# Kernel tuning notes

Hardware: AMD Instinct MI355X
Metric: run time of the kernel (lower is better)

The kernel has to match this reference:

```python
import jax, jax.numpy as jnp
import numpy as np
import math

B, N = 2, 384
TF, POS, TIME = 22, 32, 32
TPROJ = TIME + 1  # embed_fixed appends frame_mask channel
CS, CZ = 256, 128
POS_MAX, TIME_MAX = 2056.0, 10000.0
LN_EPS = 1e-5


def _index_emb(idx):
    # sinusoidal positional embedding of integer indices -> [..., POS]
    K = jnp.arange(POS // 2, dtype=jnp.float32)
    ang = idx[..., None].astype(jnp.float32) * jnp.pi / (POS_MAX ** (2.0 * K / POS))
    return jnp.concatenate([jnp.sin(ang), jnp.cos(ang)], axis=-1)


def _time_emb(t):
    # standard score-sde timestep embedding -> [M, TIME]
    half = TIME // 2
    freqs = jnp.exp(-(math.log(TIME_MAX) / (half - 1)) * jnp.arange(half, dtype=jnp.float32))
    ang = t[:, None] * freqs[None, :]
    return jnp.concatenate([jnp.sin(ang), jnp.cos(ang)], axis=-1)


def _ln(x, g, b):
    m = jnp.mean(x, axis=-1, keepdims=True)
    v = jnp.var(x, axis=-1, keepdims=True)
    return (x - m) * jax.lax.rsqrt(v + LN_EPS) * g + b


def _lin(x, W, b):
    return x @ W.T + b


def _forward(seq_idx, seq_feat, timestep, frame_mask,
             W_npos, b_npos, W_ntf, b_ntf, W_ntime, b_ntime,
             W_n1, b_n1, W_n2, b_n2, g_n, be_n,
             W_epos, b_epos, W_etf, b_etf, W_etime, b_etime,
             W_e1, b_e1, W_e2, b_e2, g_e, be_e):
    Bn, Nn = seq_idx.shape
    rel = seq_idx[:, :, None] - seq_idx[:, None, :]  # [B,N,N]
    seq_emb = _lin(_index_emb(seq_idx), W_npos, b_npos)          # [B,N,CS]
    edge_emb = _lin(_index_emb(rel), W_epos, b_epos)             # [B,N,N,CZ]
    seq_emb = seq_emb + _lin(seq_feat, W_ntf, b_ntf)
    # _cross_concat(x) @ W^T == (x @ Wl^T)[:, :, None] + (x @ Wr^T)[:, None, :] + b
    # (same math, avoids the O(N^2 * 2*TF) concatenated intermediate)
    edge_emb = edge_emb + (seq_feat @ W_etf[:, :TF].T)[:, :, None, :] \
                        + (seq_feat @ W_etf[:, TF:].T)[:, None, :, :] + b_etf
    t_res = (timestep[:, None] * frame_mask).reshape(-1)
    temb = _time_emb(t_res).reshape(Bn, Nn, TIME)
    temb = jnp.concatenate([temb, frame_mask[..., None]], axis=-1)  # embed_fixed -> TPROJ
    seq_emb = seq_emb + _lin(temb, W_ntime, b_ntime)
    edge_emb = edge_emb + (temb @ W_etime[:, :TPROJ].T)[:, :, None, :] \
                        + (temb @ W_etime[:, TPROJ:].T)[:, None, :, :] + b_etime
    # node_embedder: ReLU -> Linear -> ReLU -> Linear -> LayerNorm
    h = _lin(jax.nn.relu(seq_emb), W_n1, b_n1)
    seq_emb = _ln(_lin(jax.nn.relu(h), W_n2, b_n2), g_n, be_n)
    h = _lin(jax.nn.relu(edge_emb), W_e1, b_e1)
    edge_emb = _ln(_lin(jax.nn.relu(h), W_e2, b_e2), g_e, be_e)
    return seq_emb, edge_emb


def setup_inputs() -> dict:
    key = jax.random.key(0)
    ks = jax.random.split(key, 20)
    inp = {
        'seq_idx': jnp.sort(jax.random.randint(ks[0], (B, N), 0, 1000), axis=-1),
        'seq_feat': jax.random.normal(ks[1], (B, N, TF), dtype=jnp.float32),
        'timestep': jax.random.uniform(ks[2], (B,), dtype=jnp.float32),
        'frame_mask': jnp.ones((B, N), dtype=jnp.float32),
    }
    def lin(k, o, i):
        return 0.02 * jax.random.normal(k, (o, i), dtype=jnp.float32), jnp.zeros((o,), jnp.float32)
    inp['W_npos'], inp['b_npos'] = lin(ks[3], CS, POS)
    inp['W_ntf'], inp['b_ntf'] = lin(ks[4], CS, TF)
    inp['W_ntime'], inp['b_ntime'] = lin(ks[5], CS, TPROJ)
    inp['W_n1'], inp['b_n1'] = lin(ks[6], CS, CS)
    inp['W_n2'], inp['b_n2'] = lin(ks[7], CS, CS)
    inp['g_n'], inp['be_n'] = jnp.ones((CS,), jnp.float32), jnp.zeros((CS,), jnp.float32)
    inp['W_epos'], inp['b_epos'] = lin(ks[8], CZ, POS)
    inp['W_etf'], inp['b_etf'] = lin(ks[9], CZ, 2 * TF)
    inp['W_etime'], inp['b_etime'] = lin(ks[10], CZ, 2 * TPROJ)
    inp['W_e1'], inp['b_e1'] = lin(ks[11], CZ, CZ)
    inp['W_e2'], inp['b_e2'] = lin(ks[12], CZ, CZ)
    inp['g_e'], inp['be_e'] = jnp.ones((CZ,), jnp.float32), jnp.zeros((CZ,), jnp.float32)
    return inp


def reference(seq_idx, seq_feat, timestep, frame_mask,
              W_npos, b_npos, W_ntf, b_ntf, W_ntime, b_ntime,
              W_n1, b_n1, W_n2, b_n2, g_n, be_n,
              W_epos, b_epos, W_etf, b_etf, W_etime, b_etime,
              W_e1, b_e1, W_e2, b_e2, g_e, be_e):
    return _forward(seq_idx, seq_feat, timestep, frame_mask,
                    W_npos, b_npos, W_ntf, b_ntf, W_ntime, b_ntime,
                    W_n1, b_n1, W_n2, b_n2, g_n, be_n,
                    W_epos, b_epos, W_etf, b_etf, W_etime, b_etime,
                    W_e1, b_e1, W_e2, b_e2, g_e, be_e)
```

## Files before the change

kernel.cpp:

```cpp
#include <hip/hip_runtime.h>
#include <hip/hip_bf16.h>

#define BB 2
#define NN 384
#define TFD 22
#define POSD 32
#define TPROJ 33
#define CS 256
#define CZ 128
#define PI_F 3.14159265358979323846f

typedef __hip_bfloat16 bf16;
typedef __attribute__((ext_vector_type(8))) short short8;
typedef __attribute__((ext_vector_type(4))) float floatx4;

__device__ __forceinline__ float bfbits2f(unsigned short u) {
  unsigned v = ((unsigned)u) << 16;
  float f;
  __builtin_memcpy(&f, &v, 4);
  return f;
}
__device__ __forceinline__ unsigned short f2bf(float x) {
  bf16 h = __float2bfloat16(x);
  unsigned short u;
  __builtin_memcpy(&u, &h, 2);
  return u;
}
__device__ __forceinline__ bool probe_f32(const void* fm) {
  return *(const unsigned*)fm == 0x3F800000u;
}

#define TAB_OFF 0
#define SEQ0_OFF 262144
#define EL_OFF 458752
#define ER_OFF 557056
#define P_OFF 655360
#define WB_OFF 716288
#define pSEQF 0
#define pTS 16896
#define pFM 16898
#define pWNPOS 17666
#define pBNPOS 25858
#define pWNTF 26114
#define pBNTF 31746
#define pWNTIME 32002
#define pBNTIME 40450
#define pBN1 40706
#define pBN2 40962
#define pGN 41218
#define pBEN 41474
#define pWEPOS 41730
#define pBEPOS 45826
#define pWETF 45954
#define pBETF 51586
#define pWETIME 51714
#define pBETIME 60162
#define pBE1 60290
#define pBE2 60418
#define pGE 60546
#define pBEE 60674
#define UB_WE1 0
#define UB_WE2 16384
#define UB_WN1 32768
#define UB_WN2 98304

struct InPtrs { const void* p[28]; };

__global__ void cvt_all(InPtrs ip, float* __restrict__ ws) {
  const int idx = blockIdx.x * 256 + threadIdx.x;
  if (idx >= 224642) return;
  const int srci[27] = {1,2,3,4,5,6,7,8,9,11,13,14,15,16,17,18,19,20,21,23,25,26,27,22,24,10,12};
  const int pre[28] = {0,16896,16898,17666,25858,26114,31746,32002,40450,40706,40962,41218,41474,
                       41730,45826,45954,51586,51714,60162,60290,60418,60546,60674,60802,
                       77186,93570,159106,224642};
  const bool f32 = probe_f32(ip.p[3]);
  int e = 0;
  while (idx >= pre[e + 1]) ++e;
  const int j = idx - pre[e];
  const void* sp = ip.p[srci[e]];
  if (e < 23) {
    float v = f32 ? ((const float*)sp)[j] : bfbits2f(((const unsigned short*)sp)[j]);
    ws[P_OFF + pre[e] + j] = v;
  } else {
    const int ub[4] = {UB_WE1, UB_WE2, UB_WN1, UB_WN2};
    unsigned short* wb = (unsigned short*)(ws + WB_OFF);
    wb[ub[e - 23] + j] = f32 ? f2bf(((const float*)sp)[j]) : ((const unsigned short*)sp)[j];
  }
}

__global__ void tab_kernel(float* __restrict__ ws) {
  const float* P = ws + P_OFF;
  __shared__ float pe[POSD];
  int r = blockIdx.x, t = threadIdx.x;
  if (t < 16) {
    float ang = (float)(r - 1024) * PI_F * powf(2056.0f, -(float)t * (1.0f / 16.0f));
    pe[t] = sinf(ang);
    pe[t + 16] = cosf(ang);
  }
  __syncthreads();
  float acc = P[pBEPOS + t] + P[pBETF + t] + P[pBETIME + t];
  const float* w = P + pWEPOS + t * POSD;
#pragma unroll
  for (int k = 0; k < POSD; ++k) acc += pe[k] * w[k];
  ws[TAB_OFF + r * CZ + t] = acc;
}

__global__ void nodeprep(const int* __restrict__ seq_idx, float* __restrict__ ws) {
  const float* P = ws + P_OFF;
  __shared__ float pe[POSD];
  __shared__ float temb[TPROJ];
  __shared__ float sf[TFD];
  int bn = blockIdx.x, t = threadIdx.x;
  int b = bn / NN;
  float fm = P[pFM + bn];
  if (t < 16) {
    float idxv = (float)seq_idx[bn];
    float ang = idxv * PI_F * powf(2056.0f, -(float)t * (1.0f / 16.0f));
    pe[t] = sinf(ang);
    pe[t + 16] = cosf(ang);
    float tres = P[pTS + b] * fm;
    float freq = expf(-(logf(10000.0f) * (1.0f / 15.0f)) * (float)t);
    temb[t] = sinf(tres * freq);
    temb[t + 16] = cosf(tres * freq);
  }
  if (t == 16) temb[32] = fm;
  if (t < TFD) sf[t] = P[pSEQF + bn * TFD + t];
  __syncthreads();
  {
    int c = t;
    float acc = P[pBNPOS + c] + P[pBNTF + c] + P[pBNTIME + c];
    const float* w = P + pWNPOS + c * POSD;
#pragma unroll
    for (int k = 0; k < POSD; ++k) acc += pe[k] * w[k];
    const float* w2 = P + pWNTF + c * TFD;
#pragma unroll
    for (int k = 0; k < TFD; ++k) acc += sf[k] * w2[k];
    const float* w3 = P + pWNTIME + c * TPROJ;
#pragma unroll
    for (int k = 0; k < TPROJ; ++k) acc += temb[k] * w3[k];
    ws[SEQ0_OFF + bn * CS + c] = acc;
  }
  if (t < CZ) {
    int c = t;
    float acc = 0.0f;
    const float* w = P + pWETF + c * (2 * TFD);
#pragma unroll
    for (int k = 0; k < TFD; ++k) acc += sf[k] * w[k];
    const float* w2 = P + pWETIME + c * (2 * TPROJ);
#pragma unroll
    for (int k = 0; k < TPROJ; ++k) acc += temb[k] * w2[k];
    ws[EL_OFF + bn * CZ + c] = acc;
  } else {
    int c = t - CZ;
    float acc = 0.0f;
    const float* w = P + pWETF + c * (2 * TFD) + TFD;
#pragma unroll
    for (int k = 0; k < TFD; ++k) acc += sf[k] * w[k];
    const float* w2 = P + pWETIME + c * (2 * TPROJ) + TPROJ;
#pragma unroll
    for (int k = 0; k < TPROJ; ++k) acc += temb[k] * w2[k];
    ws[ER_OFF + bn * CZ + c] = acc;
  }
}

__global__ __launch_bounds__(256) void node_mfma(const float* __restrict__ ws,
                                                 const void* __restrict__ fmraw,
                                                 void* __restrict__ outv) {
  __shared__ __align__(16) unsigned short sA0[32][CS + 8];
  __shared__ __align__(16) unsigned short sA1[32][CS + 8];
  __shared__ float sO[32][CS + 4];
  __shared__ float sRed[32][8], sRedQ[32][8], sMu[32], sRs[32];
  const float* P = ws + P_OFF;
  const unsigned short* WB = (const unsigned short*)(ws + WB_OFF);
  const unsigned short* W1 = WB + UB_WN1;
  const unsigned short* W2 = WB + UB_WN2;
  const int row0 = blockIdx.x * 32;
  const int t = threadIdx.x;
  const int wave = t >> 6, lane = t & 63, quad = lane >> 4, l16 = lane & 15;
  {
    const float* seq0 = ws + SEQ0_OFF;
#pragma unroll
    for (int r = 0; r < 32; ++r) sA0[r][t] = f2bf(fmaxf(seq0[(row0 + r) * CS + t], 0.0f));
  }
  __syncthreads();
  short8 af[2][8];
  floatx4 acc[2][4];
#pragma unroll
  for (int mt = 0; mt < 2; ++mt)
#pragma unroll
    for (int ks = 0; ks < 8; ++ks)
      af[mt][ks] = *(const short8*)&sA0[mt * 16 + l16][ks * 32 + quad * 8];
#pragma unroll
  for (int mt = 0; mt < 2; ++mt)
#pragma unroll
    for (int n = 0; n < 4; ++n) acc[mt][n] = (floatx4){0.f, 0.f, 0.f, 0.f};
#pragma unroll
  for (int ntl = 0; ntl < 4; ++ntl) {
    int n0 = (wave * 4 + ntl) * 16;
#pragma unroll
    for (int ks = 0; ks < 8; ++ks) {
      short8 bfr = *(const short8*)&W1[(n0 + l16) * CS + ks * 32 + quad * 8];
      acc[0][ntl] = __builtin_amdgcn_mfma_f32_16x16x32_bf16(af[0][ks], bfr, acc[0][ntl], 0, 0, 0);
      acc[1][ntl] = __builtin_amdgcn_mfma_f32_16x16x32_bf16(af[1][ks], bfr, acc[1][ntl], 0, 0, 0);
    }
  }
#pragma unroll
  for (int ntl = 0; ntl < 4; ++ntl) {
    int n0 = (wave * 4 + ntl) * 16;
    float b1v = P[pBN1 + n0 + l16];
#pragma unroll
    for (int mt = 0; mt < 2; ++mt)
#pragma unroll
      for (int i = 0; i < 4; ++i)
        sA1[mt * 16 + quad * 4 + i][n0 + l16] = f2bf(fmaxf(acc[mt][ntl][i] + b1v, 0.0f));
  }
  __syncthreads();
#pragma unroll
  for (int mt = 0; mt < 2; ++mt)
#pragma unroll
    for (int ks = 0; ks < 8; ++ks)
      af[mt][ks] = *(const short8*)&sA1[mt * 16 + l16][ks * 32 + quad * 8];
#pragma unroll
  for (int mt = 0; mt < 2; ++mt)
#pragma unroll
    for (int n = 0; n < 4; ++n) acc[mt][n] = (floatx4){0.f, 0.f, 0.f, 0.f};
#pragma unroll
  for (int ntl = 0; ntl < 4; ++ntl) {
    int n0 = (wave * 4 + ntl) * 16;
#pragma unroll
    for (int ks = 0; ks < 8; ++ks) {
      short8 bfr = *(const short8*)&W2[(n0 + l16) * CS + ks * 32 + quad * 8];
      acc[0][ntl] = __builtin_amdgcn_mfma_f32_16x16x32_bf16(af[0][ks], bfr, acc[0][ntl], 0, 0, 0);
      acc[1][ntl] = __builtin_amdgcn_mfma_f32_16x16x32_bf16(af[1][ks], bfr, acc[1][ntl], 0, 0, 0);
    }
  }
#pragma unroll
  for (int ntl = 0; ntl < 4; ++ntl) {
    int n0 = (wave * 4 + ntl) * 16;
    float b2v = P[pBN2 + n0 + l16];
#pragma unroll
    for (int mt = 0; mt < 2; ++mt)
#pragma unroll
      for (int i = 0; i < 4; ++i)
        sO[mt * 16 + quad * 4 + i][n0 + l16] = acc[mt][ntl][i] + b2v;
  }
  __syncthreads();
  {
    int r = t >> 3, seg = t & 7;
    float s = 0.f, q = 0.f;
#pragma unroll
    for (int k = 0; k < 32; ++k) { float v = sO[r][seg * 32 + k]; s += v; q += v * v; }
    sRed[r][seg] = s; sRedQ[r][seg] = q;
  }
  __syncthreads();
  if (t < 32) {
    float s = 0.f, q = 0.f;
#pragma unroll
    for (int k = 0; k < 8; ++k) { s += sRed[t][k]; q += sRedQ[t][k]; }
    float mu = s * (1.0f / CS);
    float var = q * (1.0f / CS) - mu * mu;
    sMu[t] = mu; sRs[t] = rsqrtf(var + 1e-5f);
  }
  __syncthreads();
  {
    float g = P[pGN + t], be = P[pBEN + t];
    if (probe_f32(fmraw)) {
      float* o = (float*)outv;
#pragma unroll
      for (int r = 0; r < 32; ++r)
        o[(size_t)(row0 + r) * CS + t] = (sO[r][t] - sMu[r]) * sRs[r] * g + be;
    } else {
      bf16* o = (bf16*)outv;
#pragma unroll
      for (int r = 0; r < 32; ++r)
        o[(size_t)(row0 + r) * CS + t] = __float2bfloat16((sO[r][t] - sMu[r]) * sRs[r] * g + be);
    }
  }
}

__global__ __launch_bounds__(256) void edge_mfma(const int* __restrict__ seq_idx,
                                                 const float* __restrict__ ws,
                                                 const void* __restrict__ fmraw,
                                                 void* __restrict__ outv) {
  __shared__ __align__(16) unsigned short sA0[32][CZ + 8];
  __shared__ __align__(16) unsigned short sA1[32][CZ + 8];
  __shared__ float sO[32][CZ + 4];
  __shared__ int sRel[32];
  __shared__ float sRed[32][8], sRedQ[32][8], sMu[32], sRs[32];
  const float* tab = ws + TAB_OFF;
  const float* eL = ws + EL_OFF;
  const float* eR = ws + ER_OFF;
  const float* P = ws + P_OFF;
  const unsigned short* WB = (const unsigned short*)(ws + WB_OFF);
  const unsigned short* W1 = WB + UB_WE1;
  const unsigned short* W2 = WB + UB_WE2;
  const int bid = blockIdx.x;
  const int jt = bid % (NN / 32);
  const int rem = bid / (NN / 32);
  const int irow = rem % NN;
  const int b = rem / NN;
  const int j0 = jt * 32;
  const int t = threadIdx.x;
  const int wave = t >> 6, lane = t & 63, quad = lane >> 4, l16 = lane & 15;
  if (t < 32) {
    int rel = seq_idx[b * NN + irow] - seq_idx[b * NN + j0 + t] + 1024;
    sRel[t] = min(max(rel, 0), 2047);
  }
  __syncthreads();
  {
    int c = t & 127, rh = (t >> 7) * 16;
    float eLi = eL[(b * NN + irow) * CZ + c];
#pragma unroll
    for (int rr = 0; rr < 16; ++rr) {
      int r = rh + rr;
      float v = tab[sRel[r] * CZ + c] + eLi + eR[(b * NN + j0 + r) * CZ + c];
      sA0[r][c] = f2bf(fmaxf(v, 0.0f));
    }
  }
  __syncthreads();
  short8 af[2][4];
  floatx4 acc[2][2];
#pragma unroll
  for (int mt = 0; mt < 2; ++mt)
#pragma unroll
    for (int ks = 0; ks < 4; ++ks)
      af[mt][ks] = *(const short8*)&sA0[mt * 16 + l16][ks * 32 + quad * 8];
#pragma unroll
  for (int mt = 0; mt < 2; ++mt)
#pragma unroll
    for (int n = 0; n < 2; ++n) acc[mt][n] = (floatx4){0.f, 0.f, 0.f, 0.f};
#pragma unroll
  for (int ntl = 0; ntl < 2; ++ntl) {
    int n0 = (wave * 2 + ntl) * 16;
#pragma unroll
    for (int ks = 0; ks < 4; ++ks) {
      short8 bfr = *(const short8*)&W1[(n0 + l16) * CZ + ks * 32 + quad * 8];
      acc[0][ntl] = __builtin_amdgcn_mfma_f32_16x16x32_bf16(af[0][ks], bfr, acc[0][ntl], 0, 0, 0);
      acc[1][ntl] = __builtin_amdgcn_mfma_f32_16x16x32_bf16(af[1][ks], bfr, acc[1][ntl], 0, 0, 0);
    }
  }
#pragma unroll
  for (int ntl = 0; ntl < 2; ++ntl) {
    int n0 = (wave * 2 + ntl) * 16;
    float b1v = P[pBE1 + n0 + l16];
#pragma unroll
    for (int mt = 0; mt < 2; ++mt)
#pragma unroll
      for (int i = 0; i < 4; ++i)
        sA1[mt * 16 + quad * 4 + i][n0 + l16] = f2bf(fmaxf(acc[mt][ntl][i] + b1v, 0.0f));
  }
  __syncthreads();
#pragma unroll
  for (int mt = 0; mt < 2; ++mt)
#pragma unroll
    for (int ks = 0; ks < 4; ++ks)
      af[mt][ks] = *(const short8*)&sA1[mt * 16 + l16][ks * 32 + quad * 8];
#pragma unroll
  for (int mt = 0; mt < 2; ++mt)
#pragma unroll
    for (int n = 0; n < 2; ++n) acc[mt][n] = (floatx4){0.f, 0.f, 0.f, 0.f};
#pragma unroll
  for (int ntl = 0; ntl < 2; ++ntl) {
    int n0 = (wave * 2 + ntl) * 16;
#pragma unroll
    for (int ks = 0; ks < 4; ++ks) {
      short8 bfr = *(const short8*)&W2[(n0 + l16) * CZ + ks * 32 + quad * 8];
      acc[0][ntl] = __builtin_amdgcn_mfma_f32_16x16x32_bf16(af[0][ks], bfr, acc[0][ntl], 0, 0, 0);
      acc[1][ntl] = __builtin_amdgcn_mfma_f32_16x16x32_bf16(af[1][ks], bfr, acc[1][ntl], 0, 0, 0);
    }
  }
#pragma unroll
  for (int ntl = 0; ntl < 2; ++ntl) {
    int n0 = (wave * 2 + ntl) * 16;
    float b2v = P[pBE2 + n0 + l16];
#pragma unroll
    for (int mt = 0; mt < 2; ++mt)
#pragma unroll
      for (int i = 0; i < 4; ++i)
        sO[mt * 16 + quad * 4 + i][n0 + l16] = acc[mt][ntl][i] + b2v;
  }
  __syncthreads();
  {
    int r = t >> 3, seg = t & 7;
    float s = 0.f, q = 0.f;
#pragma unroll
    for (int k = 0; k < 16; ++k) { float v = sO[r][seg * 16 + k]; s += v; q += v * v; }
    sRed[r][seg] = s; sRedQ[r][seg] = q;
  }
  __syncthreads();
  if (t < 32) {
    float s = 0.f, q = 0.f;
#pragma unroll
    for (int k = 0; k < 8; ++k) { s += sRed[t][k]; q += sRedQ[t][k]; }
    float mu = s * (1.0f / CZ);
    float var = q * (1.0f / CZ) - mu * mu;
    sMu[t] = mu; sRs[t] = rsqrtf(var + 1e-5f);
  }
  __syncthreads();
  {
    int c = t & 127, rh = (t >> 7) * 16;
    float g = P[pGE + c], be = P[pBEE + c];
    size_t base = ((size_t)(b * NN + irow) * NN + j0) * CZ + c;
    if (probe_f32(fmraw)) {
      float* o = (float*)outv + (size_t)BB * NN * CS;
#pragma unroll
      for (int rr = 0; rr < 16; ++rr) {
        int r = rh + rr;
        o[base + (size_t)r * CZ] = (sO[r][c] - sMu[r]) * sRs[r] * g + be;
      }
    } else {
      bf16* o = (bf16*)outv + (size_t)BB * NN * CS;
#pragma unroll
      for (int rr = 0; rr < 16; ++rr) {
        int r = rh + rr;
        o[base + (size_t)r * CZ] = __float2bfloat16((sO[r][c] - sMu[r]) * sRs[r] * g + be);
      }
    }
  }
}

extern "C" void kernel_launch(void* const* d_in, const int* in_sizes, int n_in,
                              void* d_out, int out_size, void* d_ws, size_t ws_size,
                              hipStream_t stream) {
  (void)in_sizes; (void)n_in; (void)out_size; (void)ws_size;
  const int* seq_idx = (const int*)d_in[0];
  float* ws = (float*)d_ws;
  InPtrs ip;
  for (int i = 0; i < 28; ++i) ip.p[i] = d_in[i];
  hipLaunchKernelGGL(cvt_all, dim3(878), dim3(256), 0, stream, ip, ws);
  hipLaunchKernelGGL(tab_kernel, dim3(2048), dim3(CZ), 0, stream, ws);
  hipLaunchKernelGGL(nodeprep, dim3(BB * NN), dim3(CS), 0, stream, seq_idx, ws);
  hipLaunchKernelGGL(node_mfma, dim3(BB * NN / 32), dim3(256), 0, stream, ws, d_in[3], d_out);
  hipLaunchKernelGGL(edge_mfma, dim3(BB * NN * (NN / 32)), dim3(256), 0, stream,
                     seq_idx, ws, d_in[3], d_out);
}
```

Baseline: 306.9 us.

## Merge prep kernels and node/edge MLPs into two launches with persistent edge blocks

Collapses five launches into two. The first kernel merges parameter conversion, the relative-position table and node prep, reading raw inputs directly instead of staging a float copy first. The second kernel handles both node rows and edge rows in a shared-memory union. Edge blocks now own a whole i-row and loop over all j tiles, keeping W1/W2 fragments and biases in registers and using vectorized gathers. This cuts launch overhead and repeated weight loads, but gives fewer, longer edge blocks (768), which may lower occupancy and load balance.

Measured after the change: 306.7 us. About the same (-0.1%).

```diff
diff --git a/kernel.cpp b/kernel.cpp
--- a/kernel.cpp
+++ b/kernel.cpp
@@ -12,6 +12,7 @@
 
 typedef __hip_bfloat16 bf16;
 typedef __attribute__((ext_vector_type(8))) short short8;
+typedef __attribute__((ext_vector_type(4))) short short4v;
 typedef __attribute__((ext_vector_type(4))) float floatx4;
 
 __device__ __forceinline__ float bfbits2f(unsigned short u) {
@@ -29,391 +30,392 @@
 __device__ __forceinline__ bool probe_f32(const void* fm) {
   return *(const unsigned*)fm == 0x3F800000u;
 }
+__device__ __forceinline__ float ldf(const void* p, int j, bool f32) {
+  return f32 ? ((const float*)p)[j] : bfbits2f(((const unsigned short*)p)[j]);
+}
 
 #define TAB_OFF 0
 #define SEQ0_OFF 262144
 #define EL_OFF 458752
 #define ER_OFF 557056
-#define P_OFF 655360
-#define WB_OFF 716288
-#define pSEQF 0
-#define pTS 16896
-#define pFM 16898
-#define pWNPOS 17666
-#define pBNPOS 25858
-#define pWNTF 26114
-#define pBNTF 31746
-#define pWNTIME 32002
-#define pBNTIME 40450
-#define pBN1 40706
-#define pBN2 40962
-#define pGN 41218
-#define pBEN 41474
-#define pWEPOS 41730
-#define pBEPOS 45826
-#define pWETF 45954
-#define pBETF 51586
-#define pWETIME 51714
-#define pBETIME 60162
-#define pBE1 60290
-#define pBE2 60418
-#define pGE 60546
-#define pBEE 60674
+#define P2_OFF 655360
+#define WB_OFF 656896
+#define qBN1 0
+#define qBN2 256
+#define qGN 512
+#define qBEN 768
+#define qBE1 1024
+#define qBE2 1152
+#define qGE 1280
+#define qBEE 1408
 #define UB_WE1 0
 #define UB_WE2 16384
 #define UB_WN1 32768
 #define UB_WN2 98304
 
+#define NPREP_BLKS (BB * NN)
+#define TAB_BLKS 1024
+#define CVT_BLKS 646
+#define NODE_BLKS 48
+
 struct InPtrs { const void* p[28]; };
 
-__global__ void cvt_all(InPtrs ip, float* __restrict__ ws) {
-  const int idx = blockIdx.x * 256 + threadIdx.x;
-  if (idx >= 224642) return;
-  const int srci[27] = {1,2,3,4,5,6,7,8,9,11,13,14,15,16,17,18,19,20,21,23,25,26,27,22,24,10,12};
-  const int pre[28] = {0,16896,16898,17666,25858,26114,31746,32002,40450,40706,40962,41218,41474,
-                       41730,45826,45954,51586,51714,60162,60290,60418,60546,60674,60802,
-                       77186,93570,159106,224642};
+__global__ __launch_bounds__(256) void prep(InPtrs ip, const int* __restrict__ seq_idx,
+                                            float* __restrict__ ws) {
   const bool f32 = probe_f32(ip.p[3]);
-  int e = 0;
-  while (idx >= pre[e + 1]) ++e;
-  const int j = idx - pre[e];
-  const void* sp = ip.p[srci[e]];
-  if (e < 23) {
-    float v = f32 ? ((const float*)sp)[j] : bfbits2f(((const unsigned short*)sp)[j]);
-    ws[P_OFF + pre[e] + j] = v;
+  const int blk = blockIdx.x;
+  const int t = threadIdx.x;
+  if (blk < NPREP_BLKS) {
+    __shared__ float pe[POSD];
+    __shared__ float temb[TPROJ];
+    __shared__ float sf[TFD];
+    const int bn = blk, b = bn / NN;
+    const float fm = ldf(ip.p[3], bn, f32);
+    if (t < 16) {
+      float idxv = (float)seq_idx[bn];
+      float ang = idxv * PI_F * powf(2056.0f, -(float)t * (1.0f / 16.0f));
+      pe[t] = sinf(ang);
+      pe[t + 16] = cosf(ang);
+      float tres = ldf(ip.p[2], b, f32) * fm;
+      float freq = expf(-(logf(10000.0f) * (1.0f / 15.0f)) * (float)t);
+      temb[t] = sinf(tres * freq);
+      temb[t + 16] = cosf(tres * freq);
+    }
+    if (t == 16) temb[32] = fm;
+    if (t < TFD) sf[t] = ldf(ip.p[1], bn * TFD + t, f32);
+    __syncthreads();
+    {
+      const int c = t;
+      float acc = ldf(ip.p[5], c, f32) + ldf(ip.p[7], c, f32) + ldf(ip.p[9], c, f32);
+#pragma unroll
+      for (int k = 0; k < POSD; ++k) acc += pe[k] * ldf(ip.p[4], c * POSD + k, f32);
+#pragma unroll
+      for (int k = 0; k < TFD; ++k) acc += sf[k] * ldf(ip.p[6], c * TFD + k, f32);
+#pragma unroll
+      for (int k = 0; k < TPROJ; ++k) acc += temb[k] * ldf(ip.p[8], c * TPROJ + k, f32);
+      ws[SEQ0_OFF + bn * CS + c] = acc;
+    }
+    if (t < CZ) {
+      const int c = t;
+      float acc = 0.0f;
+#pragma unroll
+      for (int k = 0; k < TFD; ++k) acc += sf[k] * ldf(ip.p[18], c * (2 * TFD) + k, f32);
+#pragma unroll
+      for (int k = 0; k < TPROJ; ++k) acc += temb[k] * ldf(ip.p[20], c * (2 * TPROJ) + k, f32);
+      ws[EL_OFF + bn * CZ + c] = acc;
+    } else {
+      const int c = t - CZ;
+      float acc = 0.0f;
+#pragma unroll
+      for (int k = 0; k < TFD; ++k) acc += sf[k] * ldf(ip.p[18], c * (2 * TFD) + TFD + k, f32);
+#pragma unroll
+      for (int k = 0; k < TPROJ; ++k) acc += temb[k] * ldf(ip.p[20], c * (2 * TPROJ) + TPROJ + k, f32);
+      ws[ER_OFF + bn * CZ + c] = acc;
+    }
+  } else if (blk < NPREP_BLKS + TAB_BLKS) {
+    __shared__ float spe[2][POSD];
+    const int r0 = (blk - NPREP_BLKS) * 2;
+    const int rr = t >> 7, c = t & 127;
+    if (c < 16) {
+      float ang = (float)(r0 + rr - 1024) * PI_F * powf(2056.0f, -(float)c * (1.0f / 16.0f));
+      spe[rr][c] = sinf(ang);
+      spe[rr][c + 16] = cosf(ang);
+    }
+    __syncthreads();
+    float acc = ldf(ip.p[17], c, f32) + ldf(ip.p[19], c, f32) + ldf(ip.p[21], c, f32);
+#pragma unroll
+    for (int k = 0; k < POSD; ++k) acc += spe[rr][k] * ldf(ip.p[16], c * POSD + k, f32);
+    ws[TAB_OFF + (r0 + rr) * CZ + c] = acc;
   } else {
-    const int ub[4] = {UB_WE1, UB_WE2, UB_WN1, UB_WN2};
-    unsigned short* wb = (unsigned short*)(ws + WB_OFF);
-    wb[ub[e - 23] + j] = f32 ? f2bf(((const float*)sp)[j]) : ((const unsigned short*)sp)[j];
+    const int idx = (blk - NPREP_BLKS - TAB_BLKS) * 256 + t;
+    if (idx < 1536) {
+      int src, off;
+      if (idx < 256)       { src = 11; off = idx; }
+      else if (idx < 512)  { src = 13; off = idx - 256; }
+      else if (idx < 768)  { src = 14; off = idx - 512; }
+      else if (idx < 1024) { src = 15; off = idx - 768; }
+      else if (idx < 1152) { src = 23; off = idx - 1024; }
+      else if (idx < 1280) { src = 25; off = idx - 1152; }
+      else if (idx < 1408) { src = 26; off = idx - 1280; }
+      else                 { src = 27; off = idx - 1408; }
+      ws[P2_OFF + idx] = ldf(ip.p[src], off, f32);
+    } else {
+      const int j = idx - 1536;
+      int src, loc;
+      if (j < 16384)      { src = 22; loc = j; }
+      else if (j < 32768) { src = 24; loc = j - 16384; }
+      else if (j < 98304) { src = 10; loc = j - 32768; }
+      else                { src = 12; loc = j - 98304; }
+      const void* sp = ip.p[src];
+      unsigned short* wb = (unsigned short*)(ws + WB_OFF);
+      wb[j] = f32 ? f2bf(((const float*)sp)[loc]) : ((const unsigned short*)sp)[loc];
+    }
   }
 }
 
-__global__ void tab_kernel(float* __restrict__ ws) {
-  const float* P = ws + P_OFF;
-  __shared__ float pe[POSD];
-  int r = blockIdx.x, t = threadIdx.x;
-  if (t < 16) {
-    float ang = (float)(r - 1024) * PI_F * powf(2056.0f, -(float)t * (1.0f / 16.0f));
-    pe[t] = sinf(ang);
-    pe[t + 16] = cosf(ang);
-  }
-  __syncthreads();
-  float acc = P[pBEPOS + t] + P[pBETF + t] + P[pBETIME + t];
-  const float* w = P + pWEPOS + t * POSD;
-#pragma unroll
-  for (int k = 0; k < POSD; ++k) acc += pe[k] * w[k];
-  ws[TAB_OFF + r * CZ + t] = acc;
-}
-
-__global__ void nodeprep(const int* __restrict__ seq_idx, float* __restrict__ ws) {
-  const float* P = ws + P_OFF;
-  __shared__ float pe[POSD];
-  __shared__ float temb[TPROJ];
-  __shared__ float sf[TFD];
-  int bn = blockIdx.x, t = threadIdx.x;
-  int b = bn / NN;
-  float fm = P[pFM + bn];
-  if (t < 16) {
-    float idxv = (float)seq_idx[bn];
-    float ang = idxv * PI_F * powf(2056.0f, -(float)t * (1.0f / 16.0f));
-    pe[t] = sinf(ang);
-    pe[t + 16] = cosf(ang);
-    float tres = P[pTS + b] * fm;
-    float freq = expf(-(logf(10000.0f) * (1.0f / 15.0f)) * (float)t);
-    temb[t] = sinf(tres * freq);
-    temb[t + 16] = cosf(tres * freq);
-  }
-  if (t == 16) temb[32] = fm;
-  if (t < TFD) sf[t] = P[pSEQF + bn * TFD + t];
-  __syncthreads();
-  {
-    int c = t;
-    float acc = P[pBNPOS + c] + P[pBNTF + c] + P[pBNTIME + c];
-    const float* w = P + pWNPOS + c * POSD;
-#pragma unroll
-    for (int k = 0; k < POSD; ++k) acc += pe[k] * w[k];
-    const float* w2 = P + pWNTF + c * TFD;
-#pragma unroll
-    for (int k = 0; k < TFD; ++k) acc += sf[k] * w2[k];
-    const float* w3 = P + pWNTIME + c * TPROJ;
-#pragma unroll
-    for (int k = 0; k < TPROJ; ++k) acc += temb[k] * w3[k];
-    ws[SEQ0_OFF + bn * CS + c] = acc;
-  }
-  if (t < CZ) {
-    int c = t;
-    float acc = 0.0f;
-    const float* w = P + pWETF + c * (2 * TFD);
-#pragma unroll
-    for (int k = 0; k < TFD; ++k) acc += sf[k] * w[k];
-    const float* w2 = P + pWETIME + c * (2 * TPROJ);
-#pragma unroll
-    for (int k = 0; k < TPROJ; ++k) acc += temb[k] * w2[k];
-    ws[EL_OFF + bn * CZ + c] = acc;
-  } else {
-    int c = t - CZ;
-    float acc = 0.0f;
-    const float* w = P + pWETF + c * (2 * TFD) + TFD;
-#pragma unroll
-    for (int k = 0; k < TFD; ++k) acc += sf[k] * w[k];
-    const float* w2 = P + pWETIME + c * (2 * TPROJ) + TPROJ;
-#pragma unroll
-    for (int k = 0; k < TPROJ; ++k) acc += temb[k] * w2[k];
-    ws[ER_OFF + bn * CZ + c] = acc;
-  }
-}
-
-__global__ __launch_bounds__(256) void node_mfma(const float* __restrict__ ws,
-                                                 const void* __restrict__ fmraw,
-                                                 void* __restrict__ outv) {
-  __shared__ __align__(16) unsigned short sA0[32][CS + 8];
-  __shared__ __align__(16) unsigned short sA1[32][CS + 8];
-  __shared__ float sO[32][CS + 4];
-  __shared__ float sRed[32][8], sRedQ[32][8], sMu[32], sRs[32];
-  const float* P = ws + P_OFF;
-  const unsigned short* WB = (const unsigned short*)(ws + WB_OFF);
-  const unsigned short* W1 = WB + UB_WN1;
-  const unsigned short* W2 = WB + UB_WN2;
-  const int row0 = blockIdx.x * 32;
-  const int t = threadIdx.x;
-  const int wave = t >> 6, lane = t & 63, quad = lane >> 4, l16 = lane & 15;
-  {
-    const float* seq0 = ws + SEQ0_OFF;
-#pragma unroll
-    for (int r = 0; r < 32; ++r) sA0[r][t] = f2bf(fmaxf(seq0[(row0 + r) * CS + t], 0.0f));
-  }
-  __syncthreads();
-  short8 af[2][8];
-  floatx4 acc[2][4];
-#pragma unroll
-  for (int mt = 0; mt < 2; ++mt)
-#pragma unroll
-    for (int ks = 0; ks < 8; ++ks)
-      af[mt][ks] = *(const short8*)&sA0[mt * 16 + l16][ks * 32 + quad * 8];
-#pragma unroll
-  for (int mt = 0; mt < 2; ++mt)
-#pragma unroll
-    for (int n = 0; n < 4; ++n) acc[mt][n] = (floatx4){0.f, 0.f, 0.f, 0.f};
-#pragma unroll
-  for (int ntl = 0; ntl < 4; ++ntl) {
-    int n0 = (wave * 4 + ntl) * 16;
-#pragma unroll
-    for (int ks = 0; ks < 8; ++ks) {
-      short8 bfr = *(const short8*)&W1[(n0 + l16) * CS + ks * 32 + quad * 8];
-      acc[0][ntl] = __builtin_amdgcn_mfma_f32_16x16x32_bf16(af[0][ks], bfr, acc[0][ntl], 0, 0, 0);
-      acc[1][ntl] = __builtin_amdgcn_mfma_f32_16x16x32_bf16(af[1][ks], bfr, acc[1][ntl], 0, 0, 0);
-    }
-  }
-#pragma unroll
-  for (int ntl = 0; ntl < 4; ++ntl) {
-    int n0 = (wave * 4 + ntl) * 16;
-    float b1v = P[pBN1 + n0 + l16];
-#pragma unroll
-    for (int mt = 0; mt < 2; ++mt)
-#pragma unroll
-      for (int i = 0; i < 4; ++i)
-        sA1[mt * 16 + quad * 4 + i][n0 + l16] = f2bf(fmaxf(acc[mt][ntl][i] + b1v, 0.0f));
-  }
-  __syncthreads();
-#pragma unroll
-  for (int mt = 0; mt < 2; ++mt)
-#pragma unroll
-    for (int ks = 0; ks < 8; ++ks)
-      af[mt][ks] = *(const short8*)&sA1[mt * 16 + l16][ks * 32 + quad * 8];
-#pragma unroll
-  for (int mt = 0; mt < 2; ++mt)
-#pragma unroll
-    for (int n = 0; n < 4; ++n) acc[mt][n] = (floatx4){0.f, 0.f, 0.f, 0.f};
-#pragma unroll
-  for (int ntl = 0; ntl < 4; ++ntl) {
-    int n0 = (wave * 4 + ntl) * 16;
-#pragma unroll
-    for (int ks = 0; ks < 8; ++ks) {
-      short8 bfr = *(const short8*)&W2[(n0 + l16) * CS + ks * 32 + quad * 8];
-      acc[0][ntl] = __builtin_amdgcn_mfma_f32_16x16x32_bf16(af[0][ks], bfr, acc[0][ntl], 0, 0, 0);
-      acc[1][ntl] = __builtin_amdgcn_mfma_f32_16x16x32_bf16(af[1][ks], bfr, acc[1][ntl], 0, 0, 0);
-    }
-  }
-#pragma unroll
-  for (int ntl = 0; ntl < 4; ++ntl) {
-    int n0 = (wave * 4 + ntl) * 16;
-    float b2v = P[pBN2 + n0 + l16];
-#pragma unroll
-    for (int mt = 0; mt < 2; ++mt)
-#pragma unroll
-      for (int i = 0; i < 4; ++i)
-        sO[mt * 16 + quad * 4 + i][n0 + l16] = acc[mt][ntl][i] + b2v;
-  }
-  __syncthreads();
-  {
-    int r = t >> 3, seg = t & 7;
-    float s = 0.f, q = 0.f;
-#pragma unroll
-    for (int k = 0; k < 32; ++k) { float v = sO[r][seg * 32 + k]; s += v; q += v * v; }
-    sRed[r][seg] = s; sRedQ[r][seg] = q;
-  }
-  __syncthreads();
-  if (t < 32) {
-    float s = 0.f, q = 0.f;
-#pragma unroll
-    for (int k = 0; k < 8; ++k) { s += sRed[t][k]; q += sRedQ[t][k]; }
-    float mu = s * (1.0f / CS);
-    float var = q * (1.0f / CS) - mu * mu;
-    sMu[t] = mu; sRs[t] = rsqrtf(var + 1e-5f);
-  }
-  __syncthreads();
-  {
-    float g = P[pGN + t], be = P[pBEN + t];
-    if (probe_f32(fmraw)) {
-      float* o = (float*)outv;
-#pragma unroll
-      for (int r = 0; r < 32; ++r)
-        o[(size_t)(row0 + r) * CS + t] = (sO[r][t] - sMu[r]) * sRs[r] * g + be;
-    } else {
-      bf16* o = (bf16*)outv;
-#pragma unroll
-      for (int r = 0; r < 32; ++r)
-        o[(size_t)(row0 + r) * CS + t] = __float2bfloat16((sO[r][t] - sMu[r]) * sRs[r] * g + be);
-    }
-  }
-}
-
-__global__ __launch_bounds__(256) void edge_mfma(const int* __restrict__ seq_idx,
+union SMem {
+  struct {
+    unsigned short A0[32][CZ + 8];
+    unsigned short A1[32][CZ + 8];
+    float O[32][CZ + 4];
+    int J[NN];
+    float Red[32][8];
+    float RedQ[32][8];
+    float Mu[32];
+    float Rs[32];
+  } e;
+  struct {
+    unsigned short A0[16][CS + 8];
+    unsigned short A1[16][CS + 8];
+    float O[16][CS + 4];
+    float Red[16][16];
+    float RedQ[16][16];
+    float Mu[16];
+    float Rs[16];
+  } n;
+};
+
+__global__ __launch_bounds__(256) void main_mfma(const int* __restrict__ seq_idx,
                                                  const float* __restrict__ ws,
                                                  const void* __restrict__ fmraw,
                                                  void* __restrict__ outv) {
-  __shared__ __align__(16) unsigned short sA0[32][CZ + 8];
-  __shared__ __align__(16) unsigned short sA1[32][CZ + 8];
-  __shared__ float sO[32][CZ + 4];
-  __shared__ int sRel[32];
-  __shared__ float sRed[32][8], sRedQ[32][8], sMu[32], sRs[32];
+  __shared__ __align__(16) SMem sm;
+  const int t = threadIdx.x;
+  const int wave = t >> 6, lane = t & 63, quad = lane >> 4, l16 = lane & 15;
+  const float* P2 = ws + P2_OFF;
+  const unsigned short* WB = (const unsigned short*)(ws + WB_OFF);
+  const bool f32o = probe_f32(fmraw);
+
+  if (blockIdx.x < NODE_BLKS) {
+    const int row0 = blockIdx.x * 16;
+    const unsigned short* W1 = WB + UB_WN1;
+    const unsigned short* W2 = WB + UB_WN2;
+    const float* seq0 = ws + SEQ0_OFF;
+#pragma unroll
+    for (int r = 0; r < 16; ++r)
+      sm.n.A0[r][t] = f2bf(fmaxf(seq0[(row0 + r) * CS + t], 0.0f));
+    __syncthreads();
+    short8 af[8];
+    floatx4 acc[4];
+#pragma unroll
+    for (int ks = 0; ks < 8; ++ks) af[ks] = *(const short8*)&sm.n.A0[l16][ks * 32 + quad * 8];
+#pragma unroll
+    for (int n = 0; n < 4; ++n) acc[n] = (floatx4){0.f, 0.f, 0.f, 0.f};
+#pragma unroll
+    for (int ntl = 0; ntl < 4; ++ntl) {
+      const int n0 = wave * 64 + ntl * 16;
+#pragma unroll
+      for (int ks = 0; ks < 8; ++ks) {
+        short8 bfr = *(const short8*)&W1[(n0 + l16) * CS + ks * 32 + quad * 8];
+        acc[ntl] = __builtin_amdgcn_mfma_f32_16x16x32_bf16(af[ks], bfr, acc[ntl], 0, 0, 0);
+      }
+    }
+#pragma unroll
+    for (int ntl = 0; ntl < 4; ++ntl) {
+      const int n0 = wave * 64 + ntl * 16;
+      const float b1v = P2[qBN1 + n0 + l16];
+#pragma unroll
+      for (int i = 0; i < 4; ++i)
+        sm.n.A1[quad * 4 + i][n0 + l16] = f2bf(fmaxf(acc[ntl][i] + b1v, 0.0f));
+    }
+    __syncthreads();
+#pragma unroll
+    for (int ks = 0; ks < 8; ++ks) af[ks] = *(const short8*)&sm.n.A1[l16][ks * 32 + quad * 8];
+#pragma unroll
+    for (int n = 0; n < 4; ++n) acc[n] = (floatx4){0.f, 0.f, 0.f, 0.f};
+#pragma unroll
+    for (int ntl = 0; ntl < 4; ++ntl) {
+      const int n0 = wave * 64 + ntl * 16;
+#pragma unroll
+      for (int ks = 0; ks < 8; ++ks) {
+        short8 bfr = *(const short8*)&W2[(n0 + l16) * CS + ks * 32 + quad * 8];
+        acc[ntl] = __builtin_amdgcn_mfma_f32_16x16x32_bf16(af[ks], bfr, acc[ntl], 0, 0, 0);
+      }
+    }
+#pragma unroll
+    for (int ntl = 0; ntl < 4; ++ntl) {
+      const int n0 = wave * 64 + ntl * 16;
+      const float b2v = P2[qBN2 + n0 + l16];
+#pragma unroll
+      for (int i = 0; i < 4; ++i)
+        sm.n.O[quad * 4 + i][n0 + l16] = acc[ntl][i] + b2v;
+    }
+    __syncthreads();
+    {
+      const int r = t >> 4, seg = t & 15;
+      float s = 0.f, q = 0.f;
+#pragma unroll
+      for (int k = 0; k < 16; ++k) { float v = sm.n.O[r][seg * 16 + k]; s += v; q += v * v; }
+      sm.n.Red[r][seg] = s;
+      sm.n.RedQ[r][seg] = q;
+    }
+    __syncthreads();
+    if (t < 16) {
+      float s = 0.f, q = 0.f;
+#pragma unroll
+      for (int k = 0; k < 16; ++k) { s += sm.n.Red[t][k]; q += sm.n.RedQ[t][k]; }
+      float mu = s * (1.0f / CS);
+      float var = q * (1.0f / CS) - mu * mu;
+      sm.n.Mu[t] = mu;
+      sm.n.Rs[t] = rsqrtf(var + 1e-5f);
+    }
+    __syncthreads();
+    {
+      const float g = P2[qGN + t], be = P2[qBEN + t];
+      if (f32o) {
+        float* o = (float*)outv;
+#pragma unroll
+        for (int r = 0; r < 16; ++r)
+          o[(size_t)(row0 + r) * CS + t] = (sm.n.O[r][t] - sm.n.Mu[r]) * sm.n.Rs[r] * g + be;
+      } else {
+        bf16* o = (bf16*)outv;
+#pragma unroll
+        for (int r = 0; r < 16; ++r)
+          o[(size_t)(row0 + r) * CS + t] =
+              __float2bfloat16((sm.n.O[r][t] - sm.n.Mu[r]) * sm.n.Rs[r] * g + be);
+      }
+    }
+    return;
+  }
+
+  const int eb = blockIdx.x - NODE_BLKS;
+  const int irow = eb % NN, b = eb / NN;
+  const unsigned short* W1 = WB + UB_WE1;
+  const unsigned short* W2 = WB + UB_WE2;
   const float* tab = ws + TAB_OFF;
   const float* eL = ws + EL_OFF;
   const float* eR = ws + ER_OFF;
-  const float* P = ws + P_OFF;
-  const unsigned short* WB = (const unsigned short*)(ws + WB_OFF);
-  const unsigned short* W1 = WB + UB_WE1;
-  const unsigned short* W2 = WB + UB_WE2;
-  const int bid = blockIdx.x;
-  const int jt = bid % (NN / 32);
-  const int rem = bid / (NN / 32);
-  const int irow = rem % NN;
-  const int b = rem / NN;
-  const int j0 = jt * 32;
-  const int t = threadIdx.x;
-  const int wave = t >> 6, lane = t & 63, quad = lane >> 4, l16 = lane & 15;
-  if (t < 32) {
-    int rel = seq_idx[b * NN + irow] - seq_idx[b * NN + j0 + t] + 1024;
-    sRel[t] = min(max(rel, 0), 2047);
+  short8 w1f[2][4], w2f[2][4];
+  float b1v[2], b2v[2];
+#pragma unroll
+  for (int ntl = 0; ntl < 2; ++ntl) {
+    const int n0 = (wave * 2 + ntl) * 16;
+    b1v[ntl] = P2[qBE1 + n0 + l16];
+    b2v[ntl] = P2[qBE2 + n0 + l16];
+#pragma unroll
+    for (int ks = 0; ks < 4; ++ks) {
+      w1f[ntl][ks] = *(const short8*)&W1[(n0 + l16) * CZ + ks * 32 + quad * 8];
+      w2f[ntl][ks] = *(const short8*)&W2[(n0 + l16) * CZ + ks * 32 + quad * 8];
+    }
   }
-  __syncthreads();
-  {
-    int c = t & 127, rh = (t >> 7) * 16;
-    float eLi = eL[(b * NN + irow) * CZ + c];
-#pragma unroll
-    for (int rr = 0; rr < 16; ++rr) {
-      int r = rh + rr;
-      float v = tab[sRel[r] * CZ + c] + eLi + eR[(b * NN + j0 + r) * CZ + c];
-      sA0[r][c] = f2bf(fmaxf(v, 0.0f));
-    }
-  }
-  __syncthreads();
-  short8 af[2][4];
-  floatx4 acc[2][2];
-#pragma unroll
-  for (int mt = 0; mt < 2; ++mt)
-#pragma unroll
-    for (int ks = 0; ks < 4; ++ks)
-      af[mt][ks] = *(const short8*)&sA0[mt * 16 + l16][ks * 32 + quad * 8];
-#pragma unroll
-  for (int mt = 0; mt < 2; ++mt)
-#pragma unroll
-    for (int n = 0; n < 2; ++n) acc[mt][n] = (floatx4){0.f, 0.f, 0.f, 0.f};
-#pragma unroll
-  for (int ntl = 0; ntl < 2; ++ntl) {
-    int n0 = (wave * 2 + ntl) * 16;
-#pragma unroll
-    for (int ks = 0; ks < 4; ++ks) {
-      short8 bfr = *(const short8*)&W1[(n0 + l16) * CZ + ks * 32 + quad * 8];
-      acc[0][ntl] = __builtin_amdgcn_mfma_f32_16x16x32_bf16(af[0][ks], bfr, acc[0][ntl], 0, 0, 0);
-      acc[1][ntl] = __builtin_amdgcn_mfma_f32_16x16x32_bf16(af[1][ks], bfr, acc[1][ntl], 0, 0, 0);
-    }
-  }
-#pragma unroll
-  for (int ntl = 0; ntl < 2; ++ntl) {
-    int n0 = (wave * 2 + ntl) * 16;
-    float b1v = P[pBE1 + n0 + l16];
+  for (int k = t; k < NN; k += 256) sm.e.J[k] = seq_idx[b * NN + k];
+  const int idx_i = seq_idx[b * NN + irow];
+  const int c4 = (t & 31) * 4;
+  const int rg = t >> 5;
+  const floatx4 eLv = *(const floatx4*)&eL[(b * NN + irow) * CZ + c4];
+  const int cw = t & 127;
+  const float gv = P2[qGE + cw], bev = P2[qBEE + cw];
+  const size_t base0 = ((size_t)(b * NN + irow) * NN) * CZ;
+
+  for (int jt = 0; jt < NN / 32; ++jt) {
+    const int j0 = jt * 32;
+    __syncthreads();
+#pragma unroll
+    for (int rr = 0; rr < 4; ++rr) {
+      const int r = rg + rr * 8;
+      int rel = idx_i - sm.e.J[j0 + r] + 1024;
+      rel = min(max(rel, 0), 2047);
+      const floatx4 tv = *(const floatx4*)&tab[rel * CZ + c4];
+      const floatx4 ev = *(const floatx4*)&eR[(b * NN + j0 + r) * CZ + c4];
+      short4v sv;
+      sv[0] = (short)f2bf(fmaxf(tv[0] + ev[0] + eLv[0], 0.0f));
+      sv[1] = (short)f2bf(fmaxf(tv[1] + ev[1] + eLv[1], 0.0f));
+      sv[2] = (short)f2bf(fmaxf(tv[2] + ev[2] + eLv[2], 0.0f));
+      sv[3] = (short)f2bf(fmaxf(tv[3] + ev[3] + eLv[3], 0.0f));
+      *(short4v*)&sm.e.A0[r][c4] = sv;
+    }
+    __syncthreads();
+    short8 af[2][4];
+    floatx4 acc[2][2];
 #pragma unroll
     for (int mt = 0; mt < 2; ++mt)
 #pragma unroll
-      for (int i = 0; i < 4; ++i)
-        sA1[mt * 16 + quad * 4 + i][n0 + l16] = f2bf(fmaxf(acc[mt][ntl][i] + b1v, 0.0f));
-  }
-  __syncthreads();
-#pragma unroll
-  for (int mt = 0; mt < 2; ++mt)
-#pragma unroll
-    for (int ks = 0; ks < 4; ++ks)
-      af[mt][ks] = *(const short8*)&sA1[mt * 16 + l16][ks * 32 + quad * 8];
-#pragma unroll
-  for (int mt = 0; mt < 2; ++mt)
-#pragma unroll
-    for (int n = 0; n < 2; ++n) acc[mt][n] = (floatx4){0.f, 0.f, 0.f, 0.f};
-#pragma unroll
-  for (int ntl = 0; ntl < 2; ++ntl) {
-    int n0 = (wave * 2 + ntl) * 16;
-#pragma unroll
-    for (int ks = 0; ks < 4; ++ks) {
-      short8 bfr = *(const short8*)&W2[(n0 + l16) * CZ + ks * 32 + quad * 8];
-      acc[0][ntl] = __builtin_amdgcn_mfma_f32_16x16x32_bf16(af[0][ks], bfr, acc[0][ntl], 0, 0, 0);
-      acc[1][ntl] = __builtin_amdgcn_mfma_f32_16x16x32_bf16(af[1][ks], bfr, acc[1][ntl], 0, 0, 0);
-    }
-  }
-#pragma unroll
-  for (int ntl = 0; ntl < 2; ++ntl) {
-    int n0 = (wave * 2 + ntl) * 16;
-    float b2v = P[pBE2 + n0 + l16];
+      for (int ks = 0; ks < 4; ++ks)
+        af[mt][ks] = *(const short8*)&sm.e.A0[mt * 16 + l16][ks * 32 + quad * 8];
 #pragma unroll
     for (int mt = 0; mt < 2; ++mt)
 #pragma unroll
-      for (int i = 0; i < 4; ++i)
-        sO[mt * 16 + quad * 4 + i][n0 + l16] = acc[mt][ntl][i] + b2v;
-  }
-  __syncthreads();
-  {
-    int r = t >> 3, seg = t & 7;
-    float s = 0.f, q = 0.f;
-#pragma unroll
-    for (int k = 0; k < 16; ++k) { float v = sO[r][seg * 16 + k]; s += v; q += v * v; }
-    sRed[r][seg] = s; sRedQ[r][seg] = q;
-  }
-  __syncthreads();
-  if (t < 32) {
-    float s = 0.f, q = 0.f;
-#pragma unroll
-    for (int k = 0; k < 8; ++k) { s += sRed[t][k]; q += sRedQ[t][k]; }
-    float mu = s * (1.0f / CZ);
-    float var = q * (1.0f / CZ) - mu * mu;
-    sMu[t] = mu; sRs[t] = rsqrtf(var + 1e-5f);
-  }
-  __syncthreads();
-  {
-    int c = t & 127, rh = (t >> 7) * 16;
-    float g = P[pGE + c], be = P[pBEE + c];
-    size_t base = ((size_t)(b * NN + irow) * NN + j0) * CZ + c;
-    if (probe_f32(fmraw)) {
-      float* o = (float*)outv + (size_t)BB * NN * CS;
-#pragma unroll
-      for (int rr = 0; rr < 16; ++rr) {
-        int r = rh + rr;
-        o[base + (size_t)r * CZ] = (sO[r][c] - sMu[r]) * sRs[r] * g + be;
-      }
-    } else {
-      bf16* o = (bf16*)outv + (size_t)BB * NN * CS;
-#pragma unroll
-      for (int rr = 0; rr < 16; ++rr) {
-        int r = rh + rr;
-        o[base + (size_t)r * CZ] = __float2bfloat16((sO[r][c] - sMu[r]) * sRs[r] * g + be);
+      for (int n = 0; n < 2; ++n) acc[mt][n] = (floatx4){0.f, 0.f, 0.f, 0.f};
+#pragma unroll
+    for (int ntl = 0; ntl < 2; ++ntl)
+#pragma unroll
+      for (int ks = 0; ks < 4; ++ks) {
+        acc[0][ntl] = __builtin_amdgcn_mfma_f32_16x16x32_bf16(af[0][ks], w1f[ntl][ks], acc[0][ntl], 0, 0, 0);
+        acc[1][ntl] = __builtin_amdgcn_mfma_f32_16x16x32_bf16(af[1][ks], w1f[ntl][ks], acc[1][ntl], 0, 0, 0);
+      }
+#pragma unroll
+    for (int ntl = 0; ntl < 2; ++ntl) {
+      const int n0 = (wave * 2 + ntl) * 16;
+#pragma unroll
+      for (int mt = 0; mt < 2; ++mt)
+#pragma unroll
+        for (int i = 0; i < 4; ++i)
+          sm.e.A1[mt * 16 + quad * 4 + i][n0 + l16] = f2bf(fmaxf(acc[mt][ntl][i] + b1v[ntl], 0.0f));
+    }
+    __syncthreads();
+#pragma unroll
+    for (int mt = 0; mt < 2; ++mt)
+#pragma unroll
+      for (int ks = 0; ks < 4; ++ks)
+        af[mt][ks] = *(const short8*)&sm.e.A1[mt * 16 + l16][ks * 32 + quad * 8];
+#pragma unroll
+    for (int mt = 0; mt < 2; ++mt)
+#pragma unroll
+      for (int n = 0; n < 2; ++n) acc[mt][n] = (floatx4){0.f, 0.f, 0.f, 0.f};
+#pragma unroll
+    for (int ntl = 0; ntl < 2; ++ntl)
+#pragma unroll
+      for (int ks = 0; ks < 4; ++ks) {
+        acc[0][ntl] = __builtin_amdgcn_mfma_f32_16x16x32_bf16(af[0][ks], w2f[ntl][ks], acc[0][ntl], 0, 0, 0);
+        acc[1][ntl] = __builtin_amdgcn_mfma_f32_16x16x32_bf16(af[1][ks], w2f[ntl][ks], acc[1][ntl], 0, 0, 0);
+      }
+#pragma unroll
+    for (int ntl = 0; ntl < 2; ++ntl) {
+      const int n0 = (wave * 2 + ntl) * 16;
+#pragma unroll
+      for (int mt = 0; mt < 2; ++mt)
+#pragma unroll
+        for (int i = 0; i < 4; ++i)
+          sm.e.O[mt * 16 + quad * 4 + i][n0 + l16] = acc[mt][ntl][i] + b2v[ntl];
+    }
+    __syncthreads();
+    {
+      const int r = t >> 3, seg = t & 7;
+      float s = 0.f, q = 0.f;
+#pragma unroll
+      for (int k = 0; k < 16; ++k) { float v = sm.e.O[r][seg * 16 + k]; s += v; q += v * v; }
+      sm.e.Red[r][seg] = s;
+      sm.e.RedQ[r][seg] = q;
+    }
+    __syncthreads();
+    if (t < 32) {
+      float s = 0.f, q = 0.f;
+#pragma unroll
+      for (int k = 0; k < 8; ++k) { s += sm.e.Red[t][k]; q += sm.e.RedQ[t][k]; }
+      float mu = s * (1.0f / CZ);
+      float var = q * (1.0f / CZ) - mu * mu;
+      sm.e.Mu[t] = mu;
+      sm.e.Rs[t] = rsqrtf(var + 1e-5f);
+    }
+    __syncthreads();
+    {
+      const int rh = (t >> 7) * 16;
+      const size_t base = base0 + (size_t)j0 * CZ + cw;
+      if (f32o) {
+        float* o = (float*)outv + (size_t)BB * NN * CS;
+#pragma unroll
+        for (int rr = 0; rr < 16; ++rr) {
+          const int r = rh + rr;
+          o[base + (size_t)r * CZ] = (sm.e.O[r][cw] - sm.e.Mu[r]) * sm.e.Rs[r] * gv + bev;
+        }
+      } else {
+        bf16* o = (bf16*)outv + (size_t)BB * NN * CS;
+#pragma unroll
+        for (int rr = 0; rr < 16; ++rr) {
+          const int r = rh + rr;
+          o[base + (size_t)r * CZ] =
+              __float2bfloat16((sm.e.O[r][cw] - sm.e.Mu[r]) * sm.e.Rs[r] * gv + bev);
+        }
       }
     }
   }
@@ -427,10 +429,8 @@
   float* ws = (float*)d_ws;
   InPtrs ip;
   for (int i = 0; i < 28; ++i) ip.p[i] = d_in[i];
-  hipLaunchKernelGGL(cvt_all, dim3(878), dim3(256), 0, stream, ip, ws);
-  hipLaunchKernelGGL(tab_kernel, dim3(2048), dim3(CZ), 0, stream, ws);
-  hipLaunchKernelGGL(nodeprep, dim3(BB * NN), dim3(CS), 0, stream, seq_idx, ws);
-  hipLaunchKernelGGL(node_mfma, dim3(BB * NN / 32), dim3(256), 0, stream, ws, d_in[3], d_out);
-  hipLaunchKernelGGL(edge_mfma, dim3(BB * NN * (NN / 32)), dim3(256), 0, stream,
+  hipLaunchKernelGGL(prep, dim3(NPREP_BLKS + TAB_BLKS + CVT_BLKS), dim3(256), 0, stream,
+                     ip, seq_idx, ws);
+  hipLaunchKernelGGL(main_mfma, dim3(NODE_BLKS + BB * NN), dim3(256), 0, stream,
                      seq_idx, ws, d_in[3], d_out);
 }
```
